# Performance work log

Hardware: AMD Instinct MI355X
Metric: run time of the kernel (lower is better)

## Reference

```python
import jax, jax.numpy as jnp
import numpy as np

B, S, DM, H = 2, 2048, 1024, 16
D = DM // H  # head dim = 64


def setup_inputs() -> dict:
    key = jax.random.key(0)
    k1, k2, k3, k4, k5 = jax.random.split(key, 5)
    hidden_states = jax.random.normal(k1, (B, S, DM), dtype=jnp.float32)
    attention_mask = jnp.zeros((B, 1, S, S), dtype=jnp.float32)
    position_ids = jnp.broadcast_to(jnp.arange(S, dtype=jnp.int32), (B, S))
    # nn.Linear weights stored as (out, in); x @ W.T
    Wq = jax.random.normal(k2, (DM, DM), dtype=jnp.float32) * 0.02
    Wk = jax.random.normal(k3, (DM, DM), dtype=jnp.float32) * 0.02
    Wv = jax.random.normal(k4, (DM, DM), dtype=jnp.float32) * 0.02
    return {"hidden_states": hidden_states, "attention_mask": attention_mask,
            "position_ids": position_ids, "Wq": Wq, "Wk": Wk, "Wv": Wv}


def _rotate_half(x):
    h = x.shape[-1] // 2
    return jnp.concatenate((-x[..., h:], x[..., :h]), axis=-1)


def _rope_cos_sin(position_ids, dtype):
    # inv_freq: (D/2,)
    inv_freq = 1.0 / (10000.0 ** (jnp.arange(0, D, 2, dtype=jnp.float32) / D))
    # freqs: (B, S, D/2)
    freqs = position_ids.astype(jnp.float32)[:, :, None] * inv_freq[None, None, :]
    emb = jnp.concatenate((freqs, freqs), axis=-1)  # (B, S, D)
    return jnp.cos(emb).astype(dtype), jnp.sin(emb).astype(dtype)


def reference(hidden_states, attention_mask, position_ids, Wq, Wk, Wv):
    def split_heads(x):  # (B,S,DM) -> (B,H,S,D)
        return x.reshape(B, S, H, D).transpose(0, 2, 1, 3)

    q = split_heads(hidden_states @ Wq.T)
    k = split_heads(hidden_states @ Wk.T)
    v = split_heads(hidden_states @ Wv.T)

    q = q * (D ** -0.5)

    cos, sin = _rope_cos_sin(position_ids, q.dtype)
    cos = cos[:, None, :, :]  # unsqueeze head dim -> (B,1,S,D)
    sin = sin[:, None, :, :]
    q = q * cos + _rotate_half(q) * sin
    k = k * cos + _rotate_half(k) * sin

    # (B,H,S,S)
    scores = jnp.einsum('bhqd,bhkd->bhqk', q, k) + attention_mask
    probs = jax.nn.softmax(scores.astype(jnp.float32), axis=-1).astype(q.dtype)
    ctx = jnp.einsum('bhqk,bhkd->bhqd', probs, v)  # (B,H,S,D)
    ctx = ctx.transpose(0, 2, 1, 3).reshape(B, S, DM)
    return ctx
```

## Files before the change

kernel.cpp:

```cpp
#include <hip/hip_runtime.h>
#include <math.h>

#define B  2
#define S  2048
#define DM 1024
#define H  16
#define Dh 64
#define BH (B*H)

typedef short  bf16x8 __attribute__((ext_vector_type(8)));
typedef float  f32x4  __attribute__((ext_vector_type(4)));

__device__ __forceinline__ unsigned short f2bf(float f) {
    unsigned u = __float_as_uint(f);
    u = (u + 0x7fffu + ((u >> 16) & 1u)) >> 16;
    return (unsigned short)u;
}
__device__ __forceinline__ float bf2f(unsigned short h) {
    return __uint_as_float((unsigned)h << 16);
}

__device__ __forceinline__ void gload_lds16(const unsigned short* g, unsigned short* l) {
    __builtin_amdgcn_global_load_lds(
        (const __attribute__((address_space(1))) unsigned int*)g,
        (__attribute__((address_space(3))) unsigned int*)l,
        16, 0, 0);
}

__global__ __launch_bounds__(256) void cast_kernel(const float* __restrict__ X,
                                                   const float* __restrict__ Wq,
                                                   const float* __restrict__ Wk,
                                                   const float* __restrict__ Wv,
                                                   unsigned short* __restrict__ Xb,
                                                   unsigned short* __restrict__ Wb) {
    const long c = (long)(blockIdx.x * 256 + threadIdx.x) * 4;
    const float* src;
    unsigned short* dst;
    if (c < 4194304L) {
        src = X + c;  dst = Xb + c;
    } else {
        const long c2 = c - 4194304L;
        const int  wi = (int)(c2 >> 20);
        const long r  = c2 & 1048575L;
        src = (wi == 0 ? Wq : (wi == 1 ? Wk : Wv)) + r;
        dst = Wb + c2;
    }
    const float4 v = *(const float4*)src;
    ushort4 o;
    o.x = f2bf(v.x); o.y = f2bf(v.y); o.z = f2bf(v.z); o.w = f2bf(v.w);
    *(ushort4*)dst = o;
}

__global__ __launch_bounds__(256) void qkv_gemm(const unsigned short* __restrict__ Xb,
                                                const unsigned short* __restrict__ Wb,
                                                unsigned short* __restrict__ Qb,
                                                unsigned short* __restrict__ Kb,
                                                unsigned short* __restrict__ Vb) {
    __shared__ __align__(16) unsigned short As[128 * 32];
    __shared__ __align__(16) unsigned short Bs[128 * 32];

    const int tid  = threadIdx.x;
    const int w    = tid >> 6;
    const int lane = tid & 63;
    const int col  = lane & 15;
    const int quad = lane >> 4;
    const int m0 = blockIdx.x * 128;
    const int n0 = blockIdx.y * 128;
    const int mw = (w & 1) * 64;
    const int nw = (w >> 1) * 64;

    const int srow = (lane >> 2);
    const int sk8  = (lane & 3) * 8;

    f32x4 acc[4][4] = {};

    for (int k0 = 0; k0 < 1024; k0 += 32) {
        __syncthreads();
        #pragma unroll
        for (int it = 0; it < 2; ++it) {
            const int rbase = w * 16 + it * 64;
            gload_lds16(Xb + (size_t)(m0 + rbase + srow) * 1024 + k0 + sk8,
                        &As[rbase * 32]);
            gload_lds16(Wb + (size_t)(n0 + rbase + srow) * 1024 + k0 + sk8,
                        &Bs[rbase * 32]);
        }
        __syncthreads();

        bf16x8 a[4], bb[4];
        #pragma unroll
        for (int i = 0; i < 4; ++i)
            a[i] = *(const bf16x8*)&As[(mw + i * 16 + col) * 32 + quad * 8];
        #pragma unroll
        for (int j = 0; j < 4; ++j)
            bb[j] = *(const bf16x8*)&Bs[(nw + j * 16 + col) * 32 + quad * 8];
        #pragma unroll
        for (int i = 0; i < 4; ++i)
            #pragma unroll
            for (int j = 0; j < 4; ++j)
                acc[i][j] = __builtin_amdgcn_mfma_f32_16x16x32_bf16(a[i], bb[j], acc[i][j], 0, 0, 0);
    }

    const int wsel = n0 >> 10;
    unsigned short* dp = (wsel == 0) ? Qb : ((wsel == 1) ? Kb : Vb);
    #pragma unroll
    for (int i = 0; i < 4; ++i)
        #pragma unroll
        for (int j = 0; j < 4; ++j)
            #pragma unroll
            for (int r = 0; r < 4; ++r) {
                const int m  = m0 + mw + i * 16 + quad * 4 + r;
                const int n  = n0 + nw + j * 16 + col;
                const int n1 = n & 1023;
                const int hh = n1 >> 6, d = n1 & 63;
                const int bb2 = m >> 11, ss = m & 2047;
                dp[((size_t)(bb2 * H + hh) * S + ss) * Dh + d] = f2bf(acc[i][j][r]);
            }
}

__global__ __launch_bounds__(256) void rope_kernel(unsigned short* __restrict__ Q,
                                                   unsigned short* __restrict__ K,
                                                   const int* __restrict__ pos) {
    const int idx = blockIdx.x * 256 + threadIdx.x;
    const int i = idx & 31;
    const int s = (idx >> 5) & (S - 1);
    const int h = (idx >> 16) & (H - 1);
    const int b = idx >> 20;

    const float p   = (float)pos[b * S + s];
    const float inv = exp2f(-(float)i * 0.41524101186092029f);
    float sn, cs;
    sincosf(p * inv, &sn, &cs);

    const size_t base = ((size_t)(b * H + h) * S + s) * Dh;
    const float q0 = bf2f(Q[base + i]), q1 = bf2f(Q[base + i + 32]);
    Q[base + i]      = f2bf((q0 * cs - q1 * sn) * 0.125f);
    Q[base + i + 32] = f2bf((q1 * cs + q0 * sn) * 0.125f);
    const float k0 = bf2f(K[base + i]), k1 = bf2f(K[base + i + 32]);
    K[base + i]      = f2bf(k0 * cs - k1 * sn);
    K[base + i + 32] = f2bf(k1 * cs + k0 * sn);
}

#define KSd 72
#define SHIFT_C 8.0f
#define NT (S / 64)

__global__ __launch_bounds__(256) void attn_kernel(const unsigned short* __restrict__ Q,
                                                   const unsigned short* __restrict__ K,
                                                   const unsigned short* __restrict__ V,
                                                   const float* __restrict__ mask,
                                                   float* __restrict__ out) {
    __shared__ __align__(16) unsigned short Ks[2][64 * KSd];
    __shared__ __align__(16) unsigned short Vt[2][64 * KSd];
    __shared__ __align__(16) unsigned short Ps[4 * 32 * KSd];

    const int tid  = threadIdx.x;
    const int w    = tid >> 6;
    const int lane = tid & 63;
    const int col  = lane & 15;
    const int quad = lane >> 4;
    const int bh   = blockIdx.y;
    const int b    = bh >> 4, h = bh & 15;
    const int q0   = blockIdx.x * 128;
    const int qw   = q0 + w * 32;

    const int srow = tid >> 3;
    const int sc8  = (tid & 7) * 8;

    bf16x8 qa[2][2];
    #pragma unroll
    for (int u = 0; u < 2; ++u) {
        const unsigned short* qrow = Q + ((size_t)bh * S + qw + u * 16 + col) * Dh;
        qa[u][0] = *(const bf16x8*)(qrow + quad * 8);
        qa[u][1] = *(const bf16x8*)(qrow + 32 + quad * 8);
    }

    f32x4 o[4][2] = {};
    float lsum[2] = {0.f, 0.f};
    const float* mbase = mask + (size_t)b * S * S;
    unsigned short* pw = Ps + w * 32 * KSd;

    bf16x8 kp[2], vp[2];
    #pragma unroll
    for (int cc = 0; cc < 2; ++cc) {
        const size_t g = ((size_t)bh * S + srow + cc * 32) * Dh + sc8;
        kp[cc] = *(const bf16x8*)(K + g);
        vp[cc] = *(const bf16x8*)(V + g);
    }
    #pragma unroll
    for (int cc = 0; cc < 2; ++cc) {
        const int row = srow + cc * 32;
        *(bf16x8*)&Ks[0][row * KSd + sc8] = kp[cc];
        #pragma unroll
        for (int j = 0; j < 8; ++j) {
            const int d  = sc8 + j;
            const int kk = row ^ (((d >> 3) & 7) << 3);
            Vt[0][d * KSd + kk] = ((const unsigned short*)&vp[cc])[j];
        }
    }
    __syncthreads();

    for (int kt = 0; kt < NT; ++kt) {
        const int cur = kt & 1;

        if (kt + 1 < NT) {
            #pragma unroll
            for (int cc = 0; cc < 2; ++cc) {
                const size_t g = ((size_t)bh * S + (kt + 1) * 64 + srow + cc * 32) * Dh + sc8;
                kp[cc] = *(const bf16x8*)(K + g);
                vp[cc] = *(const bf16x8*)(V + g);
            }
        }

        float4 mv[4][2];
        #pragma unroll
        for (int u = 0; u < 2; ++u)
            #pragma unroll
            for (int f = 0; f < 4; ++f)
                mv[f][u] = *(const float4*)(mbase + (size_t)(qw + u * 16 + col) * S
                                            + kt * 64 + f * 16 + quad * 4);

        f32x4 sc[4][2] = {};
        #pragma unroll
        for (int f = 0; f < 4; ++f) {
            const bf16x8 ka0 = *(const bf16x8*)&Ks[cur][(f * 16 + col) * KSd + quad * 8];
            const bf16x8 ka1 = *(const bf16x8*)&Ks[cur][(f * 16 + col) * KSd + 32 + quad * 8];
            #pragma unroll
            for (int u = 0; u < 2; ++u) {
                sc[f][u] = __builtin_amdgcn_mfma_f32_16x16x32_bf16(ka0, qa[u][0], sc[f][u], 0, 0, 0);
                sc[f][u] = __builtin_amdgcn_mfma_f32_16x16x32_bf16(ka1, qa[u][1], sc[f][u], 0, 0, 0);
            }
        }

        #pragma unroll
        for (int u = 0; u < 2; ++u) {
            #pragma unroll
            for (int f = 0; f < 4; ++f) {
                sc[f][u][0] += mv[f][u].x; sc[f][u][1] += mv[f][u].y;
                sc[f][u][2] += mv[f][u].z; sc[f][u][3] += mv[f][u].w;
            }
            #pragma unroll
            for (int f = 0; f < 4; ++f)
                #pragma unroll
                for (int r = 0; r < 4; ++r) {
                    const float pv = __expf(sc[f][u][r] - SHIFT_C);
                    sc[f][u][r] = pv;
                    lsum[u] += pv;
                }
            unsigned short* pq = pw + (u * 16 + col) * KSd;
            #pragma unroll
            for (int f = 0; f < 4; ++f) {
                const unsigned v0 = (unsigned)f2bf(sc[f][u][0]) | ((unsigned)f2bf(sc[f][u][1]) << 16);
                const unsigned v1 = (unsigned)f2bf(sc[f][u][2]) | ((unsigned)f2bf(sc[f][u][3]) << 16);
                *(uint2*)&pq[f * 16 + quad * 4] = make_uint2(v0, v1);
            }
        }

        if (kt + 1 < NT) {
            const int nxt = cur ^ 1;
            #pragma unroll
            for (int cc = 0; cc < 2; ++cc) {
                const int row = srow + cc * 32;
                *(bf16x8*)&Ks[nxt][row * KSd + sc8] = kp[cc];
                #pragma unroll
                for (int j = 0; j < 8; ++j) {
                    const int d  = sc8 + j;
                    const int kk = row ^ (((d >> 3) & 7) << 3);
                    Vt[nxt][d * KSd + kk] = ((const unsigned short*)&vp[cc])[j];
                }
            }
        }
        __threadfence_block();

        #pragma unroll
        for (int kc = 0; kc < 2; ++kc) {
            bf16x8 pb[2];
            #pragma unroll
            for (int u = 0; u < 2; ++u)
                pb[u] = *(const bf16x8*)&pw[(u * 16 + col) * KSd + kc * 32 + quad * 8];
            #pragma unroll
            for (int g = 0; g < 4; ++g) {
                const int d  = g * 16 + col;
                const int sw = (((d >> 3) & 7) << 3);
                const bf16x8 va = *(const bf16x8*)&Vt[cur][d * KSd + ((kc * 32 + quad * 8) ^ sw)];
                #pragma unroll
                for (int u = 0; u < 2; ++u)
                    o[g][u] = __builtin_amdgcn_mfma_f32_16x16x32_bf16(va, pb[u], o[g][u], 0, 0, 0);
            }
        }
        __syncthreads();
    }

    #pragma unroll
    for (int u = 0; u < 2; ++u) {
        lsum[u] += __shfl_xor(lsum[u], 16, 64);
        lsum[u] += __shfl_xor(lsum[u], 32, 64);
    }

    #pragma unroll
    for (int u = 0; u < 2; ++u) {
        const float inv = 1.f / lsum[u];
        float* op = out + ((size_t)b * S + qw + u * 16 + col) * DM + h * Dh + quad * 4;
        #pragma unroll
        for (int g = 0; g < 4; ++g) {
            float4 ov;
            ov.x = o[g][u][0] * inv; ov.y = o[g][u][1] * inv;
            ov.z = o[g][u][2] * inv; ov.w = o[g][u][3] * inv;
            *(float4*)(op + g * 16) = ov;
        }
    }
}

extern "C" void kernel_launch(void* const* d_in, const int* in_sizes, int n_in,
                              void* d_out, int out_size, void* d_ws, size_t ws_size,
                              hipStream_t stream) {
    const float* hs   = (const float*)d_in[0];
    const float* mask = (const float*)d_in[1];
    const int*   pos  = (const int*)  d_in[2];
    const float* Wq   = (const float*)d_in[3];
    const float* Wk   = (const float*)d_in[4];
    const float* Wv   = (const float*)d_in[5];
    float* out = (float*)d_out;

    unsigned short* Xb = (unsigned short*)d_ws;
    unsigned short* Wb = Xb + 4194304;
    unsigned short* Qb = Wb + 3145728;
    unsigned short* Kb = Qb + 4194304;
    unsigned short* Vb = Kb + 4194304;

    cast_kernel<<<7168, 256, 0, stream>>>(hs, Wq, Wk, Wv, Xb, Wb);
    qkv_gemm<<<dim3(32, 24), 256, 0, stream>>>(Xb, Wb, Qb, Kb, Vb);
    rope_kernel<<<8192, 256, 0, stream>>>(Qb, Kb, pos);
    attn_kernel<<<dim3(S / 128, BH), 256, 0, stream>>>(Qb, Kb, Vb, mask, out);
}
```

Measured before the change: 229.5 us.

## Fuse RoPE into QKV GEMM epilogue and store V pre-transposed

Applies rotary embedding and the query scale directly in the QKV GEMM epilogue, which removes the separate rope kernel and its read-modify-write pass over Q and K. V is now written in a (B,H,D,S) transposed layout, so the attention kernel loads V tiles with plain vector stores into LDS instead of scalar transposing stores. The fused epilogue computes sincos per row in each wave and does scattered 2-byte stores, which adds work to the GEMM. The V LDS reads no longer use the XOR swizzle and may hit more bank conflicts.

```diff
diff --git a/kernel.cpp b/kernel.cpp
--- a/kernel.cpp
+++ b/kernel.cpp
@@ -15,16 +15,6 @@
     unsigned u = __float_as_uint(f);
     u = (u + 0x7fffu + ((u >> 16) & 1u)) >> 16;
     return (unsigned short)u;
-}
-__device__ __forceinline__ float bf2f(unsigned short h) {
-    return __uint_as_float((unsigned)h << 16);
-}
-
-__device__ __forceinline__ void gload_lds16(const unsigned short* g, unsigned short* l) {
-    __builtin_amdgcn_global_load_lds(
-        (const __attribute__((address_space(1))) unsigned int*)g,
-        (__attribute__((address_space(3))) unsigned int*)l,
-        16, 0, 0);
 }
 
 __global__ __launch_bounds__(256) void cast_kernel(const float* __restrict__ X,
@@ -51,8 +41,16 @@
     *(ushort4*)dst = o;
 }
 
+__device__ __forceinline__ void gload_lds16(const unsigned short* g, unsigned short* l) {
+    __builtin_amdgcn_global_load_lds(
+        (const __attribute__((address_space(1))) unsigned int*)g,
+        (__attribute__((address_space(3))) unsigned int*)l,
+        16, 0, 0);
+}
+
 __global__ __launch_bounds__(256) void qkv_gemm(const unsigned short* __restrict__ Xb,
                                                 const unsigned short* __restrict__ Wb,
+                                                const int* __restrict__ pos,
                                                 unsigned short* __restrict__ Qb,
                                                 unsigned short* __restrict__ Kb,
                                                 unsigned short* __restrict__ Vb) {
@@ -100,44 +98,49 @@
                 acc[i][j] = __builtin_amdgcn_mfma_f32_16x16x32_bf16(a[i], bb[j], acc[i][j], 0, 0, 0);
     }
 
-    const int wsel = n0 >> 10;
-    unsigned short* dp = (wsel == 0) ? Qb : ((wsel == 1) ? Kb : Vb);
-    #pragma unroll
-    for (int i = 0; i < 4; ++i)
-        #pragma unroll
-        for (int j = 0; j < 4; ++j)
+    const int wsel   = n0 >> 10;
+    const int base64 = (n0 & 1023) + nw;
+    const int hh     = base64 >> 6;
+
+    if (wsel == 2) {
+        #pragma unroll
+        for (int i = 0; i < 4; ++i) {
+            const int ss0 = m0 + mw + i * 16 + quad * 4;
+            const int bb2 = ss0 >> 11, ss = ss0 & 2047;
+            #pragma unroll
+            for (int j = 0; j < 4; ++j) {
+                const int d = j * 16 + col;
+                ushort4 ov;
+                ov.x = f2bf(acc[i][j][0]); ov.y = f2bf(acc[i][j][1]);
+                ov.z = f2bf(acc[i][j][2]); ov.w = f2bf(acc[i][j][3]);
+                *(ushort4*)(Vb + ((size_t)(bb2 * H + hh) * Dh + d) * S + ss) = ov;
+            }
+        }
+    } else {
+        unsigned short* dp = (wsel == 0) ? Qb : Kb;
+        const float qscale = (wsel == 0) ? 0.125f : 1.0f;
+        const float inv0 = exp2f(-(float)col * 0.41524101186092029f);
+        const float inv1 = exp2f(-(float)(col + 16) * 0.41524101186092029f);
+        #pragma unroll
+        for (int i = 0; i < 4; ++i) {
             #pragma unroll
             for (int r = 0; r < 4; ++r) {
-                const int m  = m0 + mw + i * 16 + quad * 4 + r;
-                const int n  = n0 + nw + j * 16 + col;
-                const int n1 = n & 1023;
-                const int hh = n1 >> 6, d = n1 & 63;
+                const int m   = m0 + mw + i * 16 + quad * 4 + r;
                 const int bb2 = m >> 11, ss = m & 2047;
-                dp[((size_t)(bb2 * H + hh) * S + ss) * Dh + d] = f2bf(acc[i][j][r]);
-            }
-}
-
-__global__ __launch_bounds__(256) void rope_kernel(unsigned short* __restrict__ Q,
-                                                   unsigned short* __restrict__ K,
-                                                   const int* __restrict__ pos) {
-    const int idx = blockIdx.x * 256 + threadIdx.x;
-    const int i = idx & 31;
-    const int s = (idx >> 5) & (S - 1);
-    const int h = (idx >> 16) & (H - 1);
-    const int b = idx >> 20;
-
-    const float p   = (float)pos[b * S + s];
-    const float inv = exp2f(-(float)i * 0.41524101186092029f);
-    float sn, cs;
-    sincosf(p * inv, &sn, &cs);
-
-    const size_t base = ((size_t)(b * H + h) * S + s) * Dh;
-    const float q0 = bf2f(Q[base + i]), q1 = bf2f(Q[base + i + 32]);
-    Q[base + i]      = f2bf((q0 * cs - q1 * sn) * 0.125f);
-    Q[base + i + 32] = f2bf((q1 * cs + q0 * sn) * 0.125f);
-    const float k0 = bf2f(K[base + i]), k1 = bf2f(K[base + i + 32]);
-    K[base + i]      = f2bf(k0 * cs - k1 * sn);
-    K[base + i + 32] = f2bf(k1 * cs + k0 * sn);
+                const float p = (float)pos[bb2 * S + ss];
+                float sn0, cs0, sn1, cs1;
+                sincosf(p * inv0, &sn0, &cs0);
+                sincosf(p * inv1, &sn1, &cs1);
+                const float a0 = acc[i][0][r], a1 = acc[i][1][r];
+                const float a2 = acc[i][2][r], a3 = acc[i][3][r];
+                unsigned short* o = dp + ((size_t)(bb2 * H + hh) * S + ss) * Dh;
+                o[col]      = f2bf((a0 * cs0 - a2 * sn0) * qscale);
+                o[col + 16] = f2bf((a1 * cs1 - a3 * sn1) * qscale);
+                o[col + 32] = f2bf((a2 * cs0 + a0 * sn0) * qscale);
+                o[col + 48] = f2bf((a3 * cs1 + a1 * sn1) * qscale);
+            }
+        }
+    }
 }
 
 #define KSd 72
@@ -178,24 +181,20 @@
     float lsum[2] = {0.f, 0.f};
     const float* mbase = mask + (size_t)b * S * S;
     unsigned short* pw = Ps + w * 32 * KSd;
+    const unsigned short* Kbase = K + (size_t)bh * S * Dh;
+    const unsigned short* Vbase = V + (size_t)bh * Dh * S;
 
     bf16x8 kp[2], vp[2];
     #pragma unroll
     for (int cc = 0; cc < 2; ++cc) {
-        const size_t g = ((size_t)bh * S + srow + cc * 32) * Dh + sc8;
-        kp[cc] = *(const bf16x8*)(K + g);
-        vp[cc] = *(const bf16x8*)(V + g);
+        kp[cc] = *(const bf16x8*)(Kbase + (size_t)(srow + cc * 32) * Dh + sc8);
+        vp[cc] = *(const bf16x8*)(Vbase + (size_t)(srow + cc * 32) * S + sc8);
     }
     #pragma unroll
     for (int cc = 0; cc < 2; ++cc) {
         const int row = srow + cc * 32;
         *(bf16x8*)&Ks[0][row * KSd + sc8] = kp[cc];
-        #pragma unroll
-        for (int j = 0; j < 8; ++j) {
-            const int d  = sc8 + j;
-            const int kk = row ^ (((d >> 3) & 7) << 3);
-            Vt[0][d * KSd + kk] = ((const unsigned short*)&vp[cc])[j];
-        }
+        *(bf16x8*)&Vt[0][row * KSd + sc8] = vp[cc];
     }
     __syncthreads();
 
@@ -205,9 +204,8 @@
         if (kt + 1 < NT) {
             #pragma unroll
             for (int cc = 0; cc < 2; ++cc) {
-                const size_t g = ((size_t)bh * S + (kt + 1) * 64 + srow + cc * 32) * Dh + sc8;
-                kp[cc] = *(const bf16x8*)(K + g);
-                vp[cc] = *(const bf16x8*)(V + g);
+                kp[cc] = *(const bf16x8*)(Kbase + (size_t)((kt + 1) * 64 + srow + cc * 32) * Dh + sc8);
+                vp[cc] = *(const bf16x8*)(Vbase + (size_t)(srow + cc * 32) * S + (kt + 1) * 64 + sc8);
             }
         }
 
@@ -261,12 +259,7 @@
             for (int cc = 0; cc < 2; ++cc) {
                 const int row = srow + cc * 32;
                 *(bf16x8*)&Ks[nxt][row * KSd + sc8] = kp[cc];
-                #pragma unroll
-                for (int j = 0; j < 8; ++j) {
-                    const int d  = sc8 + j;
-                    const int kk = row ^ (((d >> 3) & 7) << 3);
-                    Vt[nxt][d * KSd + kk] = ((const unsigned short*)&vp[cc])[j];
-                }
+                *(bf16x8*)&Vt[nxt][row * KSd + sc8] = vp[cc];
             }
         }
         __threadfence_block();
@@ -279,9 +272,7 @@
                 pb[u] = *(const bf16x8*)&pw[(u * 16 + col) * KSd + kc * 32 + quad * 8];
             #pragma unroll
             for (int g = 0; g < 4; ++g) {
-                const int d  = g * 16 + col;
-                const int sw = (((d >> 3) & 7) << 3);
-                const bf16x8 va = *(const bf16x8*)&Vt[cur][d * KSd + ((kc * 32 + quad * 8) ^ sw)];
+                const bf16x8 va = *(const bf16x8*)&Vt[cur][(g * 16 + col) * KSd + kc * 32 + quad * 8];
                 #pragma unroll
                 for (int u = 0; u < 2; ++u)
                     o[g][u] = __builtin_amdgcn_mfma_f32_16x16x32_bf16(va, pb[u], o[g][u], 0, 0, 0);
@@ -328,7 +319,6 @@
     unsigned short* Vb = Kb + 4194304;
 
     cast_kernel<<<7168, 256, 0, stream>>>(hs, Wq, Wk, Wv, Xb, Wb);
-    qkv_gemm<<<dim3(32, 24), 256, 0, stream>>>(Xb, Wb, Qb, Kb, Vb);
-    rope_kernel<<<8192, 256, 0, stream>>>(Qb, Kb, pos);
+    qkv_gemm<<<dim3(32, 24), 256, 0, stream>>>(Xb, Wb, pos, Qb, Kb, Vb);
     attn_kernel<<<dim3(S / 128, BH), 256, 0, stream>>>(Qb, Kb, Vb, mask, out);
 }
```

Result: no change. 228.7 us (-0.3%).
